# Performance work log

Hardware: AMD Instinct MI355X
Metric: run time of the kernel (lower is better)

Reference implementation:

```python
import jax, jax.numpy as jnp
import numpy as np

N_MQ = 50000   # number of 'mq' (user/query) nodes
N_SQ = 50000   # number of 'sq' (movie/sub-query) nodes
E = 600000     # edges of type ('mq','queries','sq'); reverse edges are the flip
EL = 200000    # supervision edges for the classifier
H = 128        # hidden_channels
F_IN = 768     # raw 'sq' feature dim (movie_lin in_features)
N_LAYERS = 4


def setup_inputs() -> dict:
    key = jax.random.key(0)
    ks = jax.random.split(key, 12)
    sH = 1.0 / np.sqrt(H)
    sF = 1.0 / np.sqrt(F_IN)
    return {
        "mq_node_id": jnp.arange(N_MQ, dtype=jnp.int64) if jax.config.jax_enable_x64 else jnp.arange(N_MQ, dtype=jnp.int32),
        "sq_node_id": jnp.arange(N_SQ, dtype=jnp.int32),
        "sq_x": jax.random.normal(ks[0], (N_SQ, F_IN), jnp.float32),
        "edge_index": jax.random.randint(ks[1], (2, E), 0, N_SQ),
        "edge_label_index": jax.random.randint(ks[2], (2, EL), 0, N_SQ),
        "user_emb": jax.random.normal(ks[3], (N_MQ, H), jnp.float32) * 0.1,
        "movie_emb": jax.random.normal(ks[4], (N_SQ, H), jnp.float32) * 0.1,
        "lin_W": jax.random.normal(ks[5], (H, F_IN), jnp.float32) * sF,
        "lin_b": jnp.zeros((H,), jnp.float32),
        "Wl_s": jax.random.normal(ks[6], (N_LAYERS, H, H), jnp.float32) * sH,
        "bl_s": jnp.zeros((N_LAYERS, H), jnp.float32),
        "Wr_s": jax.random.normal(ks[7], (N_LAYERS, H, H), jnp.float32) * sH,
        "Wl_m": jax.random.normal(ks[8], (N_LAYERS, H, H), jnp.float32) * sH,
        "bl_m": jnp.zeros((N_LAYERS, H), jnp.float32),
        "Wr_m": jax.random.normal(ks[9], (N_LAYERS, H, H), jnp.float32) * sH,
    }


def _sage(x_src, x_dst, src_idx, dst_idx, Wl, bl, Wr, n_dst):
    """PyG SAGEConv (aggr='mean', root_weight=True, bias on lin_l only)."""
    msg = x_src[src_idx]                                     # [E, H] gather
    agg = jax.ops.segment_sum(msg, dst_idx, num_segments=n_dst)
    cnt = jax.ops.segment_sum(jnp.ones((src_idx.shape[0], 1), x_src.dtype),
                              dst_idx, num_segments=n_dst)
    mean = agg / jnp.maximum(cnt, 1.0)                       # mean over in-neighbors
    return mean @ Wl.T + bl + x_dst @ Wr.T


def reference(mq_node_id, sq_node_id, sq_x, edge_index, edge_label_index,
              user_emb, movie_emb, lin_W, lin_b,
              Wl_s, bl_s, Wr_s, Wl_m, bl_m, Wr_m):
    # input encoders
    x_mq = user_emb[mq_node_id]                              # [N_MQ, H]
    x_sq = sq_x @ lin_W.T + lin_b + movie_emb[sq_node_id]    # [N_SQ, H]
    src, dst = edge_index[0], edge_index[1]                  # mq -> sq; reverse is flip
    for i in range(N_LAYERS):
        new_sq = _sage(x_mq, x_sq, src, dst, Wl_s[i], bl_s[i], Wr_s[i], N_SQ)
        new_mq = _sage(x_sq, x_mq, dst, src, Wl_m[i], bl_m[i], Wr_m[i], N_MQ)
        if i == 0:  # only conv1 has ReLU in the original GNN
            new_sq = jax.nn.relu(new_sq)
            new_mq = jax.nn.relu(new_mq)
        x_mq, x_sq = new_mq, new_sq
    # dot-product classifier over supervision edges
    return (x_mq[edge_label_index[0]] * x_sq[edge_label_index[1]]).sum(axis=-1)
```

## Files before the change

### kernel.cpp

```cpp
#include <hip/hip_runtime.h>

#define H    128
#define NMQ  50000
#define NSQ  50000
#define NE   600000
#define NEL  200000
#define FIN  768
#define NLAYERS 4
#define NBLK (NSQ / 16)

typedef __attribute__((ext_vector_type(8))) short bf16x8;
typedef __attribute__((ext_vector_type(4))) float f32x4;

__device__ inline ushort f2b(float f) {
  unsigned u = __float_as_uint(f);
  u = (u + 0x7FFFu + ((u >> 16) & 1u)) >> 16;
  return (ushort)u;
}
__device__ inline float b2f(ushort h) { return __uint_as_float((unsigned)h << 16); }

__global__ void cvt_bf16(const float* __restrict__ in, ushort* __restrict__ out, int n4) {
  int i = blockIdx.x * blockDim.x + threadIdx.x;
  if (i >= n4) return;
  float4 v = ((const float4*)in)[i];
  ushort4 o;
  o.x = f2b(v.x); o.y = f2b(v.y); o.z = f2b(v.z); o.w = f2b(v.w);
  ((ushort4*)out)[i] = o;
}

__global__ void cvt_w5(const float* __restrict__ linW,
                       const float* __restrict__ Wls, const float* __restrict__ Wrs,
                       const float* __restrict__ Wlm, const float* __restrict__ Wrm,
                       ushort* olinW, ushort* oWls, ushort* oWrs, ushort* oWlm, ushort* oWrm) {
  const float* in; ushort* out; int n4;
  switch (blockIdx.y) {
    case 0: in = linW; out = olinW; n4 = H * FIN / 4; break;
    case 1: in = Wls;  out = oWls;  n4 = NLAYERS * H * H / 4; break;
    case 2: in = Wrs;  out = oWrs;  n4 = NLAYERS * H * H / 4; break;
    case 3: in = Wlm;  out = oWlm;  n4 = NLAYERS * H * H / 4; break;
    default: in = Wrm; out = oWrm;  n4 = NLAYERS * H * H / 4; break;
  }
  int i = blockIdx.x * blockDim.x + threadIdx.x;
  if (i >= n4) return;
  float4 v = ((const float4*)in)[i];
  ushort4 o;
  o.x = f2b(v.x); o.y = f2b(v.y); o.z = f2b(v.z); o.w = f2b(v.w);
  ((ushort4*)out)[i] = o;
}

__global__ __launch_bounds__(64) void encoder_mfma(
    const float* __restrict__ A, const ushort* __restrict__ Wb,
    const float* __restrict__ bias, const float* __restrict__ memb,
    ushort* __restrict__ C)
{
  int lane = threadIdx.x;
  int rowbase = blockIdx.x * 16;
  int t = lane >> 4, fr = lane & 15;
  f32x4 acc[8];
  #pragma unroll
  for (int c = 0; c < 8; ++c)
    #pragma unroll
    for (int q = 0; q < 4; ++q) acc[c][q] = 0.f;

  int arow = rowbase + fr;
  const float* Abase = A + (long)arow * FIN + t * 8;

  for (int k0 = 0; k0 < FIN; k0 += 32) {
    bf16x8 af, bfm[8];
    {
      const float* p = Abase + k0;
      float4 v0 = *(const float4*)p;
      float4 v1 = *(const float4*)(p + 4);
      ushort tmp[8];
      tmp[0] = f2b(v0.x); tmp[1] = f2b(v0.y); tmp[2] = f2b(v0.z); tmp[3] = f2b(v0.w);
      tmp[4] = f2b(v1.x); tmp[5] = f2b(v1.y); tmp[6] = f2b(v1.z); tmp[7] = f2b(v1.w);
      af = *(bf16x8*)tmp;
    }
    #pragma unroll
    for (int cc = 0; cc < 8; ++cc) {
      int col = cc * 16 + fr;
      bfm[cc] = *(const bf16x8*)(Wb + (long)col * FIN + k0 + t * 8);
    }
    #pragma unroll
    for (int cc = 0; cc < 8; ++cc)
      acc[cc] = __builtin_amdgcn_mfma_f32_16x16x32_bf16(af, bfm[cc], acc[cc], 0, 0, 0);
  }
  #pragma unroll
  for (int cc = 0; cc < 8; ++cc)
    #pragma unroll
    for (int q = 0; q < 4; ++q) {
      int row = rowbase + t * 4 + q;
      int col = cc * 16 + fr;
      float v = acc[cc][q] + bias[col] + memb[(long)row * H + col];
      C[(long)row * H + col] = f2b(v);
    }
}

__global__ __launch_bounds__(64) void fused_layer2(
    const ushort* __restrict__ xmq, const ushort* __restrict__ xsq,
    const int* __restrict__ offs_f, const int* __restrict__ csr_f,
    const int* __restrict__ offs_r, const int* __restrict__ csr_r,
    const ushort* __restrict__ Wls, const ushort* __restrict__ Wrs,
    const float* __restrict__ bls,
    const ushort* __restrict__ Wlm, const ushort* __restrict__ Wrm,
    const float* __restrict__ blm,
    ushort* __restrict__ nsq, ushort* __restrict__ nmq, int relu)
{
  __shared__ ushort mtile[16 * 128];
  int side = blockIdx.x >= NBLK;
  int bidx = side ? blockIdx.x - NBLK : blockIdx.x;
  const ushort* xg   = side ? xsq    : xmq;
  const ushort* xs   = side ? xmq    : xsq;
  const int*    offs = side ? offs_r : offs_f;
  const int*    csr  = side ? csr_r  : csr_f;
  const ushort* Wl   = side ? Wlm    : Wls;
  const ushort* Wr   = side ? Wrm    : Wrs;
  const float*  bias = side ? blm    : bls;
  ushort*       Cout = side ? nmq    : nsq;

  int lane = threadIdx.x;
  int rowbase = bidx * 16;
  int t = lane >> 4, fr = lane & 15;
  const unsigned* X = (const unsigned*)xg;

  int srow = rowbase + fr;
  bf16x8 sfrag[4];
  #pragma unroll
  for (int ks = 0; ks < 4; ++ks)
    sfrag[ks] = *(const bf16x8*)(xs + (long)srow * H + (ks * 4 + t) * 8);

  int wslot = lane >> 2;
  unsigned* mt32 = (unsigned*)mtile;
  for (int i = 0; i < 16; ++i) {
    int row = rowbase + i;
    int s = offs[row], e = offs[row + 1];
    float a0 = 0.f, a1 = 0.f;
    int j = s;
    for (; j + 8 <= e; j += 8) {
      long i0 = csr[j], i1 = csr[j+1], i2 = csr[j+2], i3 = csr[j+3];
      long i4 = csr[j+4], i5 = csr[j+5], i6 = csr[j+6], i7 = csr[j+7];
      unsigned x0 = X[i0*64+lane], x1 = X[i1*64+lane], x2 = X[i2*64+lane], x3 = X[i3*64+lane];
      unsigned x4 = X[i4*64+lane], x5 = X[i5*64+lane], x6 = X[i6*64+lane], x7 = X[i7*64+lane];
      a0 += b2f((ushort)(x0 & 0xffff)) + b2f((ushort)(x1 & 0xffff))
          + b2f((ushort)(x2 & 0xffff)) + b2f((ushort)(x3 & 0xffff))
          + b2f((ushort)(x4 & 0xffff)) + b2f((ushort)(x5 & 0xffff))
          + b2f((ushort)(x6 & 0xffff)) + b2f((ushort)(x7 & 0xffff));
      a1 += b2f((ushort)(x0 >> 16)) + b2f((ushort)(x1 >> 16))
          + b2f((ushort)(x2 >> 16)) + b2f((ushort)(x3 >> 16))
          + b2f((ushort)(x4 >> 16)) + b2f((ushort)(x5 >> 16))
          + b2f((ushort)(x6 >> 16)) + b2f((ushort)(x7 >> 16));
    }
    if (j + 4 <= e) {
      long i0 = csr[j], i1 = csr[j+1], i2 = csr[j+2], i3 = csr[j+3];
      unsigned x0 = X[i0*64+lane], x1 = X[i1*64+lane], x2 = X[i2*64+lane], x3 = X[i3*64+lane];
      a0 += b2f((ushort)(x0 & 0xffff)) + b2f((ushort)(x1 & 0xffff))
          + b2f((ushort)(x2 & 0xffff)) + b2f((ushort)(x3 & 0xffff));
      a1 += b2f((ushort)(x0 >> 16)) + b2f((ushort)(x1 >> 16))
          + b2f((ushort)(x2 >> 16)) + b2f((ushort)(x3 >> 16));
      j += 4;
    }
    for (; j < e; ++j) {
      unsigned x = X[(long)csr[j] * 64 + lane];
      a0 += b2f((ushort)(x & 0xffff));
      a1 += b2f((ushort)(x >> 16));
    }
    float inv = (e > s) ? 1.f / (float)(e - s) : 0.f;
    a0 *= inv; a1 *= inv;
    int sw = (wslot & 8) | ((wslot & 7) ^ (i & 7));
    mt32[i * 64 + sw * 4 + (lane & 3)] = (unsigned)f2b(a0) | ((unsigned)f2b(a1) << 16);
  }

  f32x4 acc[8];
  #pragma unroll
  for (int c = 0; c < 8; ++c)
    #pragma unroll
    for (int q = 0; q < 4; ++q) acc[c][q] = 0.f;

  #pragma unroll
  for (int ks = 0; ks < 4; ++ks) {
    int slot = ks * 4 + t;
    int sw = (slot & 8) | ((slot & 7) ^ (fr & 7));
    bf16x8 af = *(const bf16x8*)&mtile[fr * 128 + sw * 8];
    bf16x8 bfm[8];
    #pragma unroll
    for (int cc = 0; cc < 8; ++cc) {
      int col = cc * 16 + fr;
      bfm[cc] = *(const bf16x8*)(Wl + (long)col * H + slot * 8);
    }
    #pragma unroll
    for (int cc = 0; cc < 8; ++cc)
      acc[cc] = __builtin_amdgcn_mfma_f32_16x16x32_bf16(af, bfm[cc], acc[cc], 0, 0, 0);
  }
  #pragma unroll
  for (int ks = 0; ks < 4; ++ks) {
    int slot = ks * 4 + t;
    bf16x8 bfm[8];
    #pragma unroll
    for (int cc = 0; cc < 8; ++cc) {
      int col = cc * 16 + fr;
      bfm[cc] = *(const bf16x8*)(Wr + (long)col * H + slot * 8);
    }
    #pragma unroll
    for (int cc = 0; cc < 8; ++cc)
      acc[cc] = __builtin_amdgcn_mfma_f32_16x16x32_bf16(sfrag[ks], bfm[cc], acc[cc], 0, 0, 0);
  }
  #pragma unroll
  for (int cc = 0; cc < 8; ++cc)
    #pragma unroll
    for (int q = 0; q < 4; ++q) {
      int row = rowbase + t * 4 + q;
      int col = cc * 16 + fr;
      float v = acc[cc][q] + bias[col];
      if (relu) v = fmaxf(v, 0.f);
      Cout[(long)row * H + col] = f2b(v);
    }
}

__global__ void deg_count(const int* __restrict__ eidx, int* __restrict__ df, int* __restrict__ dr) {
  int e = blockIdx.x * blockDim.x + threadIdx.x;
  if (e >= NE) return;
  atomicAdd(dr + eidx[e], 1);
  atomicAdd(df + eidx[NE + e], 1);
}

__global__ __launch_bounds__(1024) void exscan2(
    const int* __restrict__ degf, const int* __restrict__ degr,
    int* __restrict__ offf, int* __restrict__ offr)
{
  __shared__ int wtot[16], wpre[17];
  const int* deg = blockIdx.x ? degr : degf;
  int* offs = blockIdx.x ? offr : offf;
  int n = blockIdx.x ? NMQ : NSQ;
  int tid = threadIdx.x, wid = tid >> 6, lane = tid & 63;
  int carry = 0;
  for (int base = 0; base < n; base += 1024) {
    int i = base + tid;
    int d = (i < n) ? deg[i] : 0;
    int v = d;
    #pragma unroll
    for (int s = 1; s < 64; s <<= 1) {
      int tv = __shfl_up(v, s, 64);
      if (lane >= s) v += tv;
    }
    if (lane == 63) wtot[wid] = v;
    __syncthreads();
    if (tid == 0) {
      int run = 0;
      #pragma unroll
      for (int w = 0; w < 16; ++w) { wpre[w] = run; run += wtot[w]; }
      wpre[16] = run;
    }
    __syncthreads();
    if (i < n) offs[i] = carry + wpre[wid] + v - d;
    carry += wpre[16];
  }
  if (tid == 0) offs[n] = carry;
}

__global__ void csr_fill(const int* __restrict__ eidx,
                         const int* __restrict__ offs_f, const int* __restrict__ offs_r,
                         int* __restrict__ cur_f, int* __restrict__ cur_r,
                         int* __restrict__ csr_f, int* __restrict__ csr_r) {
  int e = blockIdx.x * blockDim.x + threadIdx.x;
  if (e >= NE) return;
  int s = eidx[e], d = eidx[NE + e];
  int p = atomicAdd(cur_f + d, 1); csr_f[offs_f[d] + p] = s;
  int q = atomicAdd(cur_r + s, 1); csr_r[offs_r[s] + q] = d;
}

__global__ __launch_bounds__(256) void edge_dot_b(
    const ushort* __restrict__ xmq, const ushort* __restrict__ xsq,
    const int* __restrict__ eli, float* __restrict__ out)
{
  int wid = (blockIdx.x << 2) + (threadIdx.x >> 6);
  int lane = threadIdx.x & 63;
  if (wid >= NEL) return;
  int a = eli[wid], b = eli[NEL + wid];
  unsigned xa = ((const unsigned*)xmq)[(long)a * 64 + lane];
  unsigned xb = ((const unsigned*)xsq)[(long)b * 64 + lane];
  float p = b2f((ushort)(xa & 0xffff)) * b2f((ushort)(xb & 0xffff))
          + b2f((ushort)(xa >> 16))    * b2f((ushort)(xb >> 16));
  #pragma unroll
  for (int off = 32; off; off >>= 1) p += __shfl_down(p, off, 64);
  if (lane == 0) out[wid] = p;
}

extern "C" void kernel_launch(void* const* d_in, const int* in_sizes, int n_in,
                              void* d_out, int out_size, void* d_ws, size_t ws_size,
                              hipStream_t stream) {
  (void)in_sizes; (void)n_in; (void)out_size; (void)ws_size;
  const float* sq_x      = (const float*)d_in[2];
  const int*   eidx      = (const int*)d_in[3];
  const int*   eli       = (const int*)d_in[4];
  const float* user_emb  = (const float*)d_in[5];
  const float* movie_emb = (const float*)d_in[6];
  const float* lin_W     = (const float*)d_in[7];
  const float* lin_b     = (const float*)d_in[8];
  const float* Wl_s      = (const float*)d_in[9];
  const float* bl_s      = (const float*)d_in[10];
  const float* Wr_s      = (const float*)d_in[11];
  const float* Wl_m      = (const float*)d_in[12];
  const float* bl_m      = (const float*)d_in[13];
  const float* Wr_m      = (const float*)d_in[14];
  float* out = (float*)d_out;

  char* ws = (char*)d_ws;
  size_t off = 0;
  auto alloc = [&](size_t bytes) {
    char* p = ws + off;
    off += (bytes + 255) & ~(size_t)255;
    return p;
  };
  ushort* xmq_a = (ushort*)alloc((size_t)NMQ * H * 2);
  ushort* xmq_b = (ushort*)alloc((size_t)NMQ * H * 2);
  ushort* xsq_a = (ushort*)alloc((size_t)NSQ * H * 2);
  ushort* xsq_b = (ushort*)alloc((size_t)NSQ * H * 2);
  ushort* linWb = (ushort*)alloc((size_t)H * FIN * 2);
  ushort* Wlsb  = (ushort*)alloc((size_t)NLAYERS * H * H * 2);
  ushort* Wrsb  = (ushort*)alloc((size_t)NLAYERS * H * H * 2);
  ushort* Wlmb  = (ushort*)alloc((size_t)NLAYERS * H * H * 2);
  ushort* Wrmb  = (ushort*)alloc((size_t)NLAYERS * H * H * 2);
  int* deg_f  = (int*)alloc((size_t)NSQ * 4);
  int* deg_r  = (int*)alloc((size_t)NMQ * 4);
  int* cur_f  = (int*)alloc((size_t)NSQ * 4);
  int* cur_r  = (int*)alloc((size_t)NMQ * 4);
  int* offs_f = (int*)alloc((size_t)(NSQ + 1) * 4);
  int* offs_r = (int*)alloc((size_t)(NMQ + 1) * 4);
  int* csr_f  = (int*)alloc((size_t)NE * 4);
  int* csr_r  = (int*)alloc((size_t)NE * 4);

  hipMemsetAsync(deg_f, 0, (char*)offs_f - (char*)deg_f, stream);

  cvt_bf16<<<(NMQ * H / 4 + 255) / 256, 256, 0, stream>>>(user_emb, xmq_a, NMQ * H / 4);
  cvt_w5<<<dim3((H * FIN / 4 + 255) / 256, 5), 256, 0, stream>>>(
      lin_W, Wl_s, Wr_s, Wl_m, Wr_m, linWb, Wlsb, Wrsb, Wlmb, Wrmb);

  encoder_mfma<<<NSQ / 16, 64, 0, stream>>>(sq_x, linWb, lin_b, movie_emb, xsq_a);
  deg_count<<<(NE + 255) / 256, 256, 0, stream>>>(eidx, deg_f, deg_r);
  exscan2<<<2, 1024, 0, stream>>>(deg_f, deg_r, offs_f, offs_r);
  csr_fill<<<(NE + 255) / 256, 256, 0, stream>>>(eidx, offs_f, offs_r, cur_f, cur_r, csr_f, csr_r);

  ushort *cm = xmq_a, *cs = xsq_a, *nm = xmq_b, *ns = xsq_b;
  for (int l = 0; l < NLAYERS; ++l) {
    fused_layer2<<<2 * NBLK, 64, 0, stream>>>(cm, cs, offs_f, csr_f, offs_r, csr_r,
        Wlsb + (size_t)l * H * H, Wrsb + (size_t)l * H * H, bl_s + (size_t)l * H,
        Wlmb + (size_t)l * H * H, Wrmb + (size_t)l * H * H, bl_m + (size_t)l * H,
        ns, nm, l == 0);
    ushort* t;
    t = cm; cm = nm; nm = t;
    t = cs; cs = ns; ns = t;
  }
  edge_dot_b<<<(NEL + 3) / 4, 256, 0, stream>>>(cm, cs, eli, out);
}
```

Measured before the change: 681.9 us.

## Reorder CSR by source-range chunks and tile encoder GEMM through LDS

The CSR is rebuilt so that each 16-row destination block's edges are grouped by source-index quarter (four chunks) across the whole block rather than per row. Gathers in a block then walk source rows in roughly ascending ranges for better cache locality, using a per-edge destination row id and run-length accumulation into a shared float buffer. The single-block exclusive scan is replaced with a three-phase multi-block scan over the larger key space. The encoder GEMM now uses 128-row blocks of 256 threads, staging swizzled bf16 tiles of A and W in LDS so W is reused across rows. The cost is extra drow arrays, more shared memory and branchy flush logic in the gather loop.

```diff
diff --git a/kernel.cpp b/kernel.cpp
--- a/kernel.cpp
+++ b/kernel.cpp
@@ -8,6 +8,9 @@
 #define FIN  768
 #define NLAYERS 4
 #define NBLK (NSQ / 16)
+#define NCH  4
+#define NK   (NSQ * NCH)
+#define NSCB ((NK + 1023) / 1024)
 
 typedef __attribute__((ext_vector_type(8))) short bf16x8;
 typedef __attribute__((ext_vector_type(4))) float f32x4;
@@ -48,78 +51,115 @@
   ((ushort4*)out)[i] = o;
 }
 
-__global__ __launch_bounds__(64) void encoder_mfma(
+__global__ __launch_bounds__(256) void encoder_mfma(
     const float* __restrict__ A, const ushort* __restrict__ Wb,
     const float* __restrict__ bias, const float* __restrict__ memb,
     ushort* __restrict__ C)
 {
-  int lane = threadIdx.x;
-  int rowbase = blockIdx.x * 16;
+  __shared__ ushort As[128 * 64];
+  __shared__ ushort Ws[128 * 64];
+  int tid = threadIdx.x, wave = tid >> 6, lane = tid & 63;
+  int rowbase = blockIdx.x * 128;
   int t = lane >> 4, fr = lane & 15;
-  f32x4 acc[8];
-  #pragma unroll
-  for (int c = 0; c < 8; ++c)
-    #pragma unroll
-    for (int q = 0; q < 4; ++q) acc[c][q] = 0.f;
-
-  int arow = rowbase + fr;
-  const float* Abase = A + (long)arow * FIN + t * 8;
-
-  for (int k0 = 0; k0 < FIN; k0 += 32) {
-    bf16x8 af, bfm[8];
-    {
-      const float* p = Abase + k0;
-      float4 v0 = *(const float4*)p;
-      float4 v1 = *(const float4*)(p + 4);
+  f32x4 acc[2][8];
+  #pragma unroll
+  for (int r = 0; r < 2; ++r)
+    #pragma unroll
+    for (int c = 0; c < 8; ++c)
+      #pragma unroll
+      for (int q = 0; q < 4; ++q) acc[r][c][q] = 0.f;
+
+  for (int k0 = 0; k0 < FIN; k0 += 64) {
+    #pragma unroll
+    for (int i = 0; i < 4; ++i) {
+      int c = tid + i * 256;
+      int row = c >> 3, slot = c & 7;
+      int grow = rowbase + row;
+      float4 v0 = make_float4(0.f, 0.f, 0.f, 0.f), v1 = v0;
+      if (grow < NSQ) {
+        const float* p = A + (long)grow * FIN + k0 + slot * 8;
+        v0 = *(const float4*)p;
+        v1 = *(const float4*)(p + 4);
+      }
       ushort tmp[8];
       tmp[0] = f2b(v0.x); tmp[1] = f2b(v0.y); tmp[2] = f2b(v0.z); tmp[3] = f2b(v0.w);
       tmp[4] = f2b(v1.x); tmp[5] = f2b(v1.y); tmp[6] = f2b(v1.z); tmp[7] = f2b(v1.w);
-      af = *(bf16x8*)tmp;
-    }
-    #pragma unroll
-    for (int cc = 0; cc < 8; ++cc) {
-      int col = cc * 16 + fr;
-      bfm[cc] = *(const bf16x8*)(Wb + (long)col * FIN + k0 + t * 8);
-    }
+      *(bf16x8*)&As[row * 64 + ((slot ^ (row & 7)) << 3)] = *(bf16x8*)tmp;
+    }
+    #pragma unroll
+    for (int i = 0; i < 4; ++i) {
+      int c = tid + i * 256;
+      int wrow = c >> 3, slot = c & 7;
+      bf16x8 v = *(const bf16x8*)(Wb + (long)wrow * FIN + k0 + slot * 8);
+      *(bf16x8*)&Ws[wrow * 64 + ((slot ^ (wrow & 7)) << 3)] = v;
+    }
+    __syncthreads();
+    #pragma unroll
+    for (int ks = 0; ks < 2; ++ks) {
+      int slot = ks * 4 + t;
+      bf16x8 af[2], bfm[8];
+      #pragma unroll
+      for (int r = 0; r < 2; ++r) {
+        int row = wave * 32 + r * 16 + fr;
+        af[r] = *(const bf16x8*)&As[row * 64 + ((slot ^ (row & 7)) << 3)];
+      }
+      #pragma unroll
+      for (int cc = 0; cc < 8; ++cc) {
+        int col = cc * 16 + fr;
+        bfm[cc] = *(const bf16x8*)&Ws[col * 64 + ((slot ^ (col & 7)) << 3)];
+      }
+      #pragma unroll
+      for (int r = 0; r < 2; ++r)
+        #pragma unroll
+        for (int cc = 0; cc < 8; ++cc)
+          acc[r][cc] = __builtin_amdgcn_mfma_f32_16x16x32_bf16(af[r], bfm[cc], acc[r][cc], 0, 0, 0);
+    }
+    __syncthreads();
+  }
+  #pragma unroll
+  for (int r = 0; r < 2; ++r)
     #pragma unroll
     for (int cc = 0; cc < 8; ++cc)
-      acc[cc] = __builtin_amdgcn_mfma_f32_16x16x32_bf16(af, bfm[cc], acc[cc], 0, 0, 0);
-  }
-  #pragma unroll
-  for (int cc = 0; cc < 8; ++cc)
-    #pragma unroll
-    for (int q = 0; q < 4; ++q) {
-      int row = rowbase + t * 4 + q;
-      int col = cc * 16 + fr;
-      float v = acc[cc][q] + bias[col] + memb[(long)row * H + col];
-      C[(long)row * H + col] = f2b(v);
-    }
+      #pragma unroll
+      for (int q = 0; q < 4; ++q) {
+        int row = rowbase + wave * 32 + r * 16 + t * 4 + q;
+        if (row < NSQ) {
+          int col = cc * 16 + fr;
+          float v = acc[r][cc][q] + bias[col] + memb[(long)row * H + col];
+          C[(long)row * H + col] = f2b(v);
+        }
+      }
 }
 
 __global__ __launch_bounds__(64) void fused_layer2(
     const ushort* __restrict__ xmq, const ushort* __restrict__ xsq,
-    const int* __restrict__ offs_f, const int* __restrict__ csr_f,
-    const int* __restrict__ offs_r, const int* __restrict__ csr_r,
+    const int* __restrict__ offs2_f, const int* __restrict__ csr_f,
+    const int* __restrict__ drow_f,
+    const int* __restrict__ offs2_r, const int* __restrict__ csr_r,
+    const int* __restrict__ drow_r,
     const ushort* __restrict__ Wls, const ushort* __restrict__ Wrs,
     const float* __restrict__ bls,
     const ushort* __restrict__ Wlm, const ushort* __restrict__ Wrm,
     const float* __restrict__ blm,
     ushort* __restrict__ nsq, ushort* __restrict__ nmq, int relu)
 {
+  __shared__ float facc[16 * 128];
   __shared__ ushort mtile[16 * 128];
   int side = blockIdx.x >= NBLK;
   int bidx = side ? blockIdx.x - NBLK : blockIdx.x;
-  const ushort* xg   = side ? xsq    : xmq;
-  const ushort* xs   = side ? xmq    : xsq;
-  const int*    offs = side ? offs_r : offs_f;
-  const int*    csr  = side ? csr_r  : csr_f;
-  const ushort* Wl   = side ? Wlm    : Wls;
-  const ushort* Wr   = side ? Wrm    : Wrs;
-  const float*  bias = side ? blm    : bls;
-  ushort*       Cout = side ? nmq    : nsq;
+  const ushort* xg    = side ? xsq     : xmq;
+  const ushort* xs    = side ? xmq     : xsq;
+  const int*    offs2 = side ? offs2_r : offs2_f;
+  const int*    csr   = side ? csr_r   : csr_f;
+  const int*    drow  = side ? drow_r  : drow_f;
+  const ushort* Wl    = side ? Wlm     : Wls;
+  const ushort* Wr    = side ? Wrm     : Wrs;
+  const float*  bias  = side ? blm     : bls;
+  ushort*       Cout  = side ? nmq     : nsq;
 
   int lane = threadIdx.x;
   int rowbase = bidx * 16;
+  int tk = bidx * 64;
   int t = lane >> 4, fr = lane & 15;
   const unsigned* X = (const unsigned*)xg;
 
@@ -128,46 +168,66 @@
   #pragma unroll
   for (int ks = 0; ks < 4; ++ks)
     sfrag[ks] = *(const bf16x8*)(xs + (long)srow * H + (ks * 4 + t) * 8);
+
+  #pragma unroll
+  for (int i = 0; i < 32; ++i) facc[i * 64 + lane] = 0.f;
+
+  float a0 = 0.f, a1 = 0.f;
+  int cur = -1;
+#define FLUSHA() do { if (cur >= 0) {                                       \
+    facc[cur * 128 + lane * 2]     += a0;                                   \
+    facc[cur * 128 + lane * 2 + 1] += a1;                                   \
+    a0 = 0.f; a1 = 0.f; } } while (0)
+
+  for (int c = 0; c < NCH; ++c) {
+    int js = offs2[tk + c * 16], je = offs2[tk + c * 16 + 16];
+    int j = js;
+    for (; j + 8 <= je; j += 8) {
+      long i0 = csr[j], i1 = csr[j+1], i2 = csr[j+2], i3 = csr[j+3];
+      long i4 = csr[j+4], i5 = csr[j+5], i6 = csr[j+6], i7 = csr[j+7];
+      int r0 = drow[j], r1 = drow[j+1], r2 = drow[j+2], r3 = drow[j+3];
+      int r4 = drow[j+4], r5 = drow[j+5], r6 = drow[j+6], r7 = drow[j+7];
+      unsigned x0 = X[i0*64+lane], x1 = X[i1*64+lane], x2 = X[i2*64+lane], x3 = X[i3*64+lane];
+      unsigned x4 = X[i4*64+lane], x5 = X[i5*64+lane], x6 = X[i6*64+lane], x7 = X[i7*64+lane];
+      if (r0 != cur) { FLUSHA(); cur = r0; }
+      a0 += b2f((ushort)(x0 & 0xffff)); a1 += b2f((ushort)(x0 >> 16));
+      if (r1 != cur) { FLUSHA(); cur = r1; }
+      a0 += b2f((ushort)(x1 & 0xffff)); a1 += b2f((ushort)(x1 >> 16));
+      if (r2 != cur) { FLUSHA(); cur = r2; }
+      a0 += b2f((ushort)(x2 & 0xffff)); a1 += b2f((ushort)(x2 >> 16));
+      if (r3 != cur) { FLUSHA(); cur = r3; }
+      a0 += b2f((ushort)(x3 & 0xffff)); a1 += b2f((ushort)(x3 >> 16));
+      if (r4 != cur) { FLUSHA(); cur = r4; }
+      a0 += b2f((ushort)(x4 & 0xffff)); a1 += b2f((ushort)(x4 >> 16));
+      if (r5 != cur) { FLUSHA(); cur = r5; }
+      a0 += b2f((ushort)(x5 & 0xffff)); a1 += b2f((ushort)(x5 >> 16));
+      if (r6 != cur) { FLUSHA(); cur = r6; }
+      a0 += b2f((ushort)(x6 & 0xffff)); a1 += b2f((ushort)(x6 >> 16));
+      if (r7 != cur) { FLUSHA(); cur = r7; }
+      a0 += b2f((ushort)(x7 & 0xffff)); a1 += b2f((ushort)(x7 >> 16));
+    }
+    for (; j < je; ++j) {
+      int r = drow[j];
+      unsigned x = X[(long)csr[j] * 64 + lane];
+      if (r != cur) { FLUSHA(); cur = r; }
+      a0 += b2f((ushort)(x & 0xffff)); a1 += b2f((ushort)(x >> 16));
+    }
+  }
+  FLUSHA();
+#undef FLUSHA
 
   int wslot = lane >> 2;
   unsigned* mt32 = (unsigned*)mtile;
   for (int i = 0; i < 16; ++i) {
-    int row = rowbase + i;
-    int s = offs[row], e = offs[row + 1];
-    float a0 = 0.f, a1 = 0.f;
-    int j = s;
-    for (; j + 8 <= e; j += 8) {
-      long i0 = csr[j], i1 = csr[j+1], i2 = csr[j+2], i3 = csr[j+3];
-      long i4 = csr[j+4], i5 = csr[j+5], i6 = csr[j+6], i7 = csr[j+7];
-      unsigned x0 = X[i0*64+lane], x1 = X[i1*64+lane], x2 = X[i2*64+lane], x3 = X[i3*64+lane];
-      unsigned x4 = X[i4*64+lane], x5 = X[i5*64+lane], x6 = X[i6*64+lane], x7 = X[i7*64+lane];
-      a0 += b2f((ushort)(x0 & 0xffff)) + b2f((ushort)(x1 & 0xffff))
-          + b2f((ushort)(x2 & 0xffff)) + b2f((ushort)(x3 & 0xffff))
-          + b2f((ushort)(x4 & 0xffff)) + b2f((ushort)(x5 & 0xffff))
-          + b2f((ushort)(x6 & 0xffff)) + b2f((ushort)(x7 & 0xffff));
-      a1 += b2f((ushort)(x0 >> 16)) + b2f((ushort)(x1 >> 16))
-          + b2f((ushort)(x2 >> 16)) + b2f((ushort)(x3 >> 16))
-          + b2f((ushort)(x4 >> 16)) + b2f((ushort)(x5 >> 16))
-          + b2f((ushort)(x6 >> 16)) + b2f((ushort)(x7 >> 16));
-    }
-    if (j + 4 <= e) {
-      long i0 = csr[j], i1 = csr[j+1], i2 = csr[j+2], i3 = csr[j+3];
-      unsigned x0 = X[i0*64+lane], x1 = X[i1*64+lane], x2 = X[i2*64+lane], x3 = X[i3*64+lane];
-      a0 += b2f((ushort)(x0 & 0xffff)) + b2f((ushort)(x1 & 0xffff))
-          + b2f((ushort)(x2 & 0xffff)) + b2f((ushort)(x3 & 0xffff));
-      a1 += b2f((ushort)(x0 >> 16)) + b2f((ushort)(x1 >> 16))
-          + b2f((ushort)(x2 >> 16)) + b2f((ushort)(x3 >> 16));
-      j += 4;
-    }
-    for (; j < e; ++j) {
-      unsigned x = X[(long)csr[j] * 64 + lane];
-      a0 += b2f((ushort)(x & 0xffff));
-      a1 += b2f((ushort)(x >> 16));
-    }
-    float inv = (e > s) ? 1.f / (float)(e - s) : 0.f;
-    a0 *= inv; a1 *= inv;
+    int deg = 0;
+    #pragma unroll
+    for (int c = 0; c < NCH; ++c)
+      deg += offs2[tk + c * 16 + i + 1] - offs2[tk + c * 16 + i];
+    float inv = deg > 0 ? 1.f / (float)deg : 0.f;
+    float b0 = facc[i * 128 + lane * 2] * inv;
+    float b1 = facc[i * 128 + lane * 2 + 1] * inv;
     int sw = (wslot & 8) | ((wslot & 7) ^ (i & 7));
-    mt32[i * 64 + sw * 4 + (lane & 3)] = (unsigned)f2b(a0) | ((unsigned)f2b(a1) << 16);
+    mt32[i * 64 + sw * 4 + (lane & 3)] = (unsigned)f2b(b0) | ((unsigned)f2b(b1) << 16);
   }
 
   f32x4 acc[8];
@@ -216,56 +276,104 @@
     }
 }
 
-__global__ void deg_count(const int* __restrict__ eidx, int* __restrict__ df, int* __restrict__ dr) {
-  int e = blockIdx.x * blockDim.x + threadIdx.x;
-  if (e >= NE) return;
-  atomicAdd(dr + eidx[e], 1);
-  atomicAdd(df + eidx[NE + e], 1);
-}
-
-__global__ __launch_bounds__(1024) void exscan2(
-    const int* __restrict__ degf, const int* __restrict__ degr,
-    int* __restrict__ offf, int* __restrict__ offr)
-{
-  __shared__ int wtot[16], wpre[17];
-  const int* deg = blockIdx.x ? degr : degf;
-  int* offs = blockIdx.x ? offr : offf;
-  int n = blockIdx.x ? NMQ : NSQ;
-  int tid = threadIdx.x, wid = tid >> 6, lane = tid & 63;
-  int carry = 0;
-  for (int base = 0; base < n; base += 1024) {
-    int i = base + tid;
-    int d = (i < n) ? deg[i] : 0;
-    int v = d;
-    #pragma unroll
-    for (int s = 1; s < 64; s <<= 1) {
-      int tv = __shfl_up(v, s, 64);
-      if (lane >= s) v += tv;
-    }
-    if (lane == 63) wtot[wid] = v;
-    __syncthreads();
-    if (tid == 0) {
-      int run = 0;
-      #pragma unroll
-      for (int w = 0; w < 16; ++w) { wpre[w] = run; run += wtot[w]; }
-      wpre[16] = run;
-    }
-    __syncthreads();
-    if (i < n) offs[i] = carry + wpre[wid] + v - d;
-    carry += wpre[16];
-  }
-  if (tid == 0) offs[n] = carry;
-}
-
-__global__ void csr_fill(const int* __restrict__ eidx,
-                         const int* __restrict__ offs_f, const int* __restrict__ offs_r,
-                         int* __restrict__ cur_f, int* __restrict__ cur_r,
-                         int* __restrict__ csr_f, int* __restrict__ csr_r) {
+__global__ void deg_count(const int* __restrict__ eidx, int* __restrict__ d2f, int* __restrict__ d2r) {
   int e = blockIdx.x * blockDim.x + threadIdx.x;
   if (e >= NE) return;
   int s = eidx[e], d = eidx[NE + e];
-  int p = atomicAdd(cur_f + d, 1); csr_f[offs_f[d] + p] = s;
-  int q = atomicAdd(cur_r + s, 1); csr_r[offs_r[s] + q] = d;
+  atomicAdd(d2f + ((d >> 4) * 64 + (s / 12500) * 16 + (d & 15)), 1);
+  atomicAdd(d2r + ((s >> 4) * 64 + (d / 12500) * 16 + (s & 15)), 1);
+}
+
+__global__ __launch_bounds__(1024) void scan_p1(
+    const int* __restrict__ d2f, const int* __restrict__ d2r,
+    int* __restrict__ bsf, int* __restrict__ bsr)
+{
+  const int* deg = blockIdx.y ? d2r : d2f;
+  int* bs = blockIdx.y ? bsr : bsf;
+  __shared__ int wt[16];
+  int i = blockIdx.x * 1024 + threadIdx.x;
+  int d = i < NK ? deg[i] : 0;
+  #pragma unroll
+  for (int s = 32; s; s >>= 1) d += __shfl_down(d, s, 64);
+  int wid = threadIdx.x >> 6, lane = threadIdx.x & 63;
+  if (lane == 0) wt[wid] = d;
+  __syncthreads();
+  if (threadIdx.x == 0) {
+    int s = 0;
+    #pragma unroll
+    for (int w = 0; w < 16; ++w) s += wt[w];
+    bs[blockIdx.x] = s;
+  }
+}
+
+__global__ __launch_bounds__(256) void scan_p2(
+    const int* __restrict__ bsf, const int* __restrict__ bsr,
+    int* __restrict__ bpf, int* __restrict__ bpr,
+    int* __restrict__ offf, int* __restrict__ offr)
+{
+  const int* bs = blockIdx.x ? bsr : bsf;
+  int* bp = blockIdx.x ? bpr : bpf;
+  int* offs = blockIdx.x ? offr : offf;
+  __shared__ int wt[4], wp[5];
+  int tid = threadIdx.x, wid = tid >> 6, lane = tid & 63;
+  int d = tid < NSCB ? bs[tid] : 0;
+  int v = d;
+  #pragma unroll
+  for (int s = 1; s < 64; s <<= 1) { int tv = __shfl_up(v, s, 64); if (lane >= s) v += tv; }
+  if (lane == 63) wt[wid] = v;
+  __syncthreads();
+  if (tid == 0) {
+    int r = 0;
+    for (int w = 0; w < 4; ++w) { wp[w] = r; r += wt[w]; }
+    wp[4] = r;
+  }
+  __syncthreads();
+  if (tid < NSCB) bp[tid] = wp[wid] + v - d;
+  if (tid == 0) offs[NK] = wp[4];
+}
+
+__global__ __launch_bounds__(1024) void scan_p3(
+    const int* __restrict__ d2f, const int* __restrict__ d2r,
+    const int* __restrict__ bpf, const int* __restrict__ bpr,
+    int* __restrict__ offf, int* __restrict__ offr)
+{
+  const int* deg = blockIdx.y ? d2r : d2f;
+  const int* bp  = blockIdx.y ? bpr : bpf;
+  int* offs = blockIdx.y ? offr : offf;
+  __shared__ int wt[16], wp[17];
+  int tid = threadIdx.x, wid = tid >> 6, lane = tid & 63;
+  int i = blockIdx.x * 1024 + tid;
+  int d = i < NK ? deg[i] : 0;
+  int v = d;
+  #pragma unroll
+  for (int s = 1; s < 64; s <<= 1) { int tv = __shfl_up(v, s, 64); if (lane >= s) v += tv; }
+  if (lane == 63) wt[wid] = v;
+  __syncthreads();
+  if (tid == 0) {
+    int r = 0;
+    for (int w = 0; w < 16; ++w) { wp[w] = r; r += wt[w]; }
+    wp[16] = r;
+  }
+  __syncthreads();
+  if (i < NK) offs[i] = bp[blockIdx.x] + wp[wid] + v - d;
+}
+
+__global__ void csr_fill(const int* __restrict__ eidx,
+                         const int* __restrict__ offs2_f, const int* __restrict__ offs2_r,
+                         int* __restrict__ cur_f, int* __restrict__ cur_r,
+                         int* __restrict__ csr_f, int* __restrict__ csr_r,
+                         int* __restrict__ drow_f, int* __restrict__ drow_r) {
+  int e = blockIdx.x * blockDim.x + threadIdx.x;
+  if (e >= NE) return;
+  int s = eidx[e], d = eidx[NE + e];
+  int kf = (d >> 4) * 64 + (s / 12500) * 16 + (d & 15);
+  int p = atomicAdd(cur_f + kf, 1);
+  int pf = offs2_f[kf] + p;
+  csr_f[pf] = s; drow_f[pf] = d & 15;
+  int kr = (s >> 4) * 64 + (d / 12500) * 16 + (s & 15);
+  int q = atomicAdd(cur_r + kr, 1);
+  int pr = offs2_r[kr] + q;
+  csr_r[pr] = d; drow_r[pr] = s & 15;
 }
 
 __global__ __launch_bounds__(256) void edge_dot_b(
@@ -320,29 +428,39 @@
   ushort* Wrsb  = (ushort*)alloc((size_t)NLAYERS * H * H * 2);
   ushort* Wlmb  = (ushort*)alloc((size_t)NLAYERS * H * H * 2);
   ushort* Wrmb  = (ushort*)alloc((size_t)NLAYERS * H * H * 2);
-  int* deg_f  = (int*)alloc((size_t)NSQ * 4);
-  int* deg_r  = (int*)alloc((size_t)NMQ * 4);
-  int* cur_f  = (int*)alloc((size_t)NSQ * 4);
-  int* cur_r  = (int*)alloc((size_t)NMQ * 4);
-  int* offs_f = (int*)alloc((size_t)(NSQ + 1) * 4);
-  int* offs_r = (int*)alloc((size_t)(NMQ + 1) * 4);
+  int* d2_f   = (int*)alloc((size_t)NK * 4);
+  int* d2_r   = (int*)alloc((size_t)NK * 4);
+  int* cur_f  = (int*)alloc((size_t)NK * 4);
+  int* cur_r  = (int*)alloc((size_t)NK * 4);
+  int* offs2_f = (int*)alloc((size_t)(NK + 1) * 4);
+  int* offs2_r = (int*)alloc((size_t)(NK + 1) * 4);
+  int* bs_f   = (int*)alloc((size_t)NSCB * 4);
+  int* bs_r   = (int*)alloc((size_t)NSCB * 4);
+  int* bp_f   = (int*)alloc((size_t)NSCB * 4);
+  int* bp_r   = (int*)alloc((size_t)NSCB * 4);
   int* csr_f  = (int*)alloc((size_t)NE * 4);
   int* csr_r  = (int*)alloc((size_t)NE * 4);
-
-  hipMemsetAsync(deg_f, 0, (char*)offs_f - (char*)deg_f, stream);
+  int* drow_f = (int*)alloc((size_t)NE * 4);
+  int* drow_r = (int*)alloc((size_t)NE * 4);
+
+  (void)hipMemsetAsync(d2_f, 0, (char*)offs2_f - (char*)d2_f, stream);
 
   cvt_bf16<<<(NMQ * H / 4 + 255) / 256, 256, 0, stream>>>(user_emb, xmq_a, NMQ * H / 4);
   cvt_w5<<<dim3((H * FIN / 4 + 255) / 256, 5), 256, 0, stream>>>(
       lin_W, Wl_s, Wr_s, Wl_m, Wr_m, linWb, Wlsb, Wrsb, Wlmb, Wrmb);
 
-  encoder_mfma<<<NSQ / 16, 64, 0, stream>>>(sq_x, linWb, lin_b, movie_emb, xsq_a);
-  deg_count<<<(NE + 255) / 256, 256, 0, stream>>>(eidx, deg_f, deg_r);
-  exscan2<<<2, 1024, 0, stream>>>(deg_f, deg_r, offs_f, offs_r);
-  csr_fill<<<(NE + 255) / 256, 256, 0, stream>>>(eidx, offs_f, offs_r, cur_f, cur_r, csr_f, csr_r);
+  encoder_mfma<<<(NSQ + 127) / 128, 256, 0, stream>>>(sq_x, linWb, lin_b, movie_emb, xsq_a);
+  deg_count<<<(NE + 255) / 256, 256, 0, stream>>>(eidx, d2_f, d2_r);
+  scan_p1<<<dim3(NSCB, 2), 1024, 0, stream>>>(d2_f, d2_r, bs_f, bs_r);
+  scan_p2<<<2, 256, 0, stream>>>(bs_f, bs_r, bp_f, bp_r, offs2_f, offs2_r);
+  scan_p3<<<dim3(NSCB, 2), 1024, 0, stream>>>(d2_f, d2_r, bp_f, bp_r, offs2_f, offs2_r);
+  csr_fill<<<(NE + 255) / 256, 256, 0, stream>>>(eidx, offs2_f, offs2_r, cur_f, cur_r,
+                                                 csr_f, csr_r, drow_f, drow_r);
 
   ushort *cm = xmq_a, *cs = xsq_a, *nm = xmq_b, *ns = xsq_b;
   for (int l = 0; l < NLAYERS; ++l) {
-    fused_layer2<<<2 * NBLK, 64, 0, stream>>>(cm, cs, offs_f, csr_f, offs_r, csr_r,
+    fused_layer2<<<2 * NBLK, 64, 0, stream>>>(cm, cs,
+        offs2_f, csr_f, drow_f, offs2_r, csr_r, drow_r,
         Wlsb + (size_t)l * H * H, Wrsb + (size_t)l * H * H, bl_s + (size_t)l * H,
         Wlmb + (size_t)l * H * H, Wrmb + (size_t)l * H * H, bl_m + (size_t)l * H,
         ns, nm, l == 0);
```

Result: slower. 1.019 ms (+49.4%).
